# Kernel optimization log

Hardware: AMD Instinct MI355X
Metric: run time of the kernel (lower is better)

Reference implementation:

```python
import jax, jax.numpy as jnp
import numpy as np

N = 4096
IN_F = 512
OUT_F = 64
HEADS = 4
ALPHA = 0.2  # leaky relu slope
NEG_INF = -9e15


def setup_inputs() -> dict:
    key = jax.random.key(0)
    k1, k2, k3, k4 = jax.random.split(key, 4)
    x = jax.random.normal(k1, (N, IN_F), dtype=jnp.float32)
    adj = jax.random.randint(k2, (N, N), 0, 2, dtype=jnp.int32)
    # xavier-uniform-like init for params
    limW = float(np.sqrt(6.0 / (IN_F + OUT_F * HEADS)))
    W = jax.random.uniform(k3, (IN_F, OUT_F * HEADS), dtype=jnp.float32, minval=-limW, maxval=limW)
    lima = float(np.sqrt(6.0 / (2 * OUT_F + 1)))
    a = jax.random.uniform(k4, (2 * OUT_F, 1), dtype=jnp.float32, minval=-lima, maxval=lima)
    return {"x": x, "adj": adj, "W": W, "a": a}


def reference(x, adj, W, a):
    # h: [N, H, F]
    h = (x @ W).reshape(N, HEADS, OUT_F)
    a_src = a[:OUT_F, 0]   # [F]
    a_dst = a[OUT_F:, 0]   # [F]
    s = jnp.einsum("nhf,f->nh", h, a_src)  # source-node score [N, H]
    t = jnp.einsum("nhf,f->nh", h, a_dst)  # dest-node score   [N, H]
    # e[i, j, k] = leaky_relu(s[i,k] + t[j,k]) -> [N, N, H]
    e = jax.nn.leaky_relu(s[:, None, :] + t[None, :, :], negative_slope=ALPHA)
    mask = (adj > 0)[:, :, None]  # [N, N, 1]
    e = jnp.where(mask, e, NEG_INF)
    attn = jax.nn.softmax(e, axis=1)  # softmax over neighbors j
    # weighted aggregation per head: [N, H, F]
    h_prime = jnp.einsum("ijh,jhf->ihf", attn, h)
    return h_prime.reshape(N, HEADS * OUT_F)
```

## Files before the change

### kernel.cpp

```cpp
#include <hip/hip_runtime.h>
#include <hip/hip_bf16.h>


#define NN 4096
#define KF 512
#define NF 256

typedef __attribute__((ext_vector_type(8))) short bf16x8;
typedef __attribute__((ext_vector_type(4))) short s16x4;
typedef __attribute__((ext_vector_type(4))) float f32x4;

union AB8 { bf16x8 v; short2 h[4]; short s[8]; int4 i4; };
union ST4 { s16x4 v; short2 h[2]; };

__device__ __forceinline__ short f2bf(float f) {
    union { float f; unsigned u; } v; v.f = f;
    unsigned r = v.u + 0x7fffu + ((v.u >> 16) & 1u);
    return (short)(r >> 16);
}
__device__ __forceinline__ float bf2f(short b) {
    union { unsigned u; float f; } v;
    v.u = ((unsigned)(unsigned short)b) << 16;
    return v.f;
}
__device__ __forceinline__ short2 pkbf(float a, float b) {
    __hip_bfloat162 t = __float22bfloat162_rn(make_float2(a, b));
    union { __hip_bfloat162 v; short2 s; } u; u.v = t;
    return u.s;
}

__global__ __launch_bounds__(256) void xcast(const float* __restrict__ x,
                                             short* __restrict__ xb) {
    int idx = (blockIdx.x * 256 + threadIdx.x) * 4;
    float4 v = *(const float4*)(x + idx);
    ST4 o; o.h[0] = pkbf(v.x, v.y); o.h[1] = pkbf(v.z, v.w);
    *(s16x4*)(xb + idx) = o.v;
}

__global__ __launch_bounds__(256) void wpack(const float* __restrict__ W,
                                             short* __restrict__ WtF) {
    int tid = blockIdx.x * 256 + threadIdx.x;
    int l = tid & 63, nt = (tid >> 6) & 3, hd = (tid >> 8) & 3, kblk = tid >> 10;
    int q = l >> 4, r = l & 15;
    int col = hd * 64 + nt * 16 + r;
    int k0 = kblk * 32 + q * 8;
    AB8 o;
    #pragma unroll
    for (int e = 0; e < 8; e++) o.s[e] = f2bf(W[(k0 + e) * NF + col]);
    *(bf16x8*)(WtF + (size_t)tid * 8) = o.v;
}

__global__ __launch_bounds__(256) void adjpack(const int* __restrict__ adj,
                                               unsigned* __restrict__ pT) {
    int gw   = (blockIdx.x * 256 + threadIdx.x) >> 6;
    int lane = threadIdx.x & 63;
    int i = gw >> 4, seg = gw & 15;
    const int* ap = adj + (size_t)i * NN + seg * 256 + lane;
    unsigned long long b0 = __ballot(ap[0]   != 0);
    unsigned long long b1 = __ballot(ap[64]  != 0);
    unsigned long long b2 = __ballot(ap[128] != 0);
    unsigned long long b3 = __ballot(ap[192] != 0);
    if (lane == 0) {
        *(uint4*)(pT + ((size_t)(seg * 2    ) * NN + i) * 4) =
            make_uint4((unsigned)b0, (unsigned)(b0 >> 32), (unsigned)b1, (unsigned)(b1 >> 32));
        *(uint4*)(pT + ((size_t)(seg * 2 + 1) * NN + i) * 4) =
            make_uint4((unsigned)b2, (unsigned)(b2 >> 32), (unsigned)b3, (unsigned)(b3 >> 32));
    }
}

__global__ __launch_bounds__(256) void gemm(const short* __restrict__ xb,
                                            const short* __restrict__ WtF,
                                            short* __restrict__ VtF) {
    const int lane = threadIdx.x & 63, wv = threadIdx.x >> 6;
    const int q = lane >> 4, r = lane & 15;
    const int i0 = blockIdx.x * 64 + wv * 16;
    const int hd = blockIdx.y >> 1, ntp = (blockIdx.y & 1) * 2;

    const short* xp = xb + (size_t)(i0 + r) * KF + q * 8;
    const short* wp = WtF + ((size_t)((hd * 4 + ntp) * 64 + lane)) * 8;

    f32x4 acc0 = {}, acc1 = {};
    #pragma unroll
    for (int kb = 0; kb < 16; kb++) {
        bf16x8 av = *(const bf16x8*)(xp + kb * 32);
        bf16x8 b0 = *(const bf16x8*)(wp + kb * 8192);
        bf16x8 b1 = *(const bf16x8*)(wp + kb * 8192 + 512);
        acc0 = __builtin_amdgcn_mfma_f32_16x16x32_bf16(av, b0, acc0, 0, 0, 0);
        acc1 = __builtin_amdgcn_mfma_f32_16x16x32_bf16(av, b1, acc1, 0, 0, 0);
    }
    const int jblk = i0 >> 5;
    const int base = (i0 & 16) + q * 4;
    const int qa = base >> 3, e0 = base & 7;
    ST4 s0, s1;
    s0.h[0] = pkbf(acc0[0], acc0[1]); s0.h[1] = pkbf(acc0[2], acc0[3]);
    s1.h[0] = pkbf(acc1[0], acc1[1]); s1.h[1] = pkbf(acc1[2], acc1[3]);
    *(s16x4*)(VtF + ((size_t)(((jblk * 4 + hd) * 4 + ntp    ) * 64 + qa * 16 + r)) * 8 + e0) = s0.v;
    *(s16x4*)(VtF + ((size_t)(((jblk * 4 + hd) * 4 + ntp + 1) * 64 + qa * 16 + r)) * 8 + e0) = s1.v;
}

__global__ __launch_bounds__(256) void prep(const short* __restrict__ VtF,
                                            const float* __restrict__ a,
                                            float* __restrict__ ipk,
                                            float2* __restrict__ jpk) {
    const int l = threadIdx.x & 63, hd = threadIdx.x >> 6;
    const int q = l >> 4, r = l & 15;
    const int jblk = blockIdx.x;
    float as[4], at[4];
    #pragma unroll
    for (int nt = 0; nt < 4; nt++) { as[nt] = a[nt * 16 + r]; at[nt] = a[64 + nt * 16 + r]; }
    float ps[8] = {}, pt[8] = {};
    #pragma unroll
    for (int nt = 0; nt < 4; nt++) {
        AB8 hv; hv.v = *(const bf16x8*)(VtF + ((size_t)(((jblk * 4 + hd) * 4 + nt) * 64 + l)) * 8);
        #pragma unroll
        for (int e = 0; e < 8; e++) { float v = bf2f(hv.s[e]); ps[e] += v * as[nt]; pt[e] += v * at[nt]; }
    }
    #pragma unroll
    for (int d = 1; d < 16; d <<= 1) {
        #pragma unroll
        for (int e = 0; e < 8; e++) { ps[e] += __shfl_xor(ps[e], d, 64); pt[e] += __shfl_xor(pt[e], d, 64); }
    }
    if (r == 0) {
        #pragma unroll
        for (int e = 0; e < 8; e++) {
            int j = jblk * 32 + q * 8 + e;
            ipk[hd * NN + j] = __expf(-0.8f * ps[e]);
            jpk[hd * NN + j] = make_float2(__expf(pt[e]), __expf(0.2f * pt[e]));
        }
    }
}

struct PF { float4 ja, jb, jc, jd; int4 v0, v1, v2, v3; };

__global__ __launch_bounds__(1024) __attribute__((amdgpu_waves_per_eu(1, 4)))
void gat_attn(const uint4* __restrict__ pT4, const float* __restrict__ ipk,
              const float* __restrict__ jpkf, const short* __restrict__ VtF,
              float* __restrict__ out) {
    const int tid = threadIdx.x, lane = tid & 63, wv = tid >> 6;
    const int hd = wv & 3, jq = wv >> 2;
    const int q = lane >> 4, r = lane & 15;
    const int i0 = blockIdx.x * 16, i = i0 + r;
    const float ci = ipk[hd * NN + i];
    const int qs = q * 8;
    const float* jpf = jpkf + (size_t)hd * NN * 2;

    f32x4 acc[5] = {};
    AB8 ones;
    #pragma unroll
    for (int e = 0; e < 8; e++) ones.s[e] = (short)0x3F80;

    auto load_pf = [&](PF& p, int it) {
        const float4* jp = (const float4*)(jpf + 2 * ((jq << 10) + (it << 5) + qs));
        p.ja = jp[0]; p.jb = jp[1]; p.jc = jp[2]; p.jd = jp[3];
        const int4* vp = (const int4*)(VtF + (size_t)(((jq * 32 + it) * 16 + hd * 4) * 512) + lane * 8);
        p.v0 = vp[0]; p.v1 = vp[64]; p.v2 = vp[128]; p.v3 = vp[192];
    };
    auto consume = [&](const PF& p, unsigned w) {
        float p0 = (w & 1u)   ? fmaxf(p.ja.x, ci * p.ja.y) : 0.f;
        float p1 = (w & 2u)   ? fmaxf(p.ja.z, ci * p.ja.w) : 0.f;
        float p2 = (w & 4u)   ? fmaxf(p.jb.x, ci * p.jb.y) : 0.f;
        float p3 = (w & 8u)   ? fmaxf(p.jb.z, ci * p.jb.w) : 0.f;
        float p4 = (w & 16u)  ? fmaxf(p.jc.x, ci * p.jc.y) : 0.f;
        float p5 = (w & 32u)  ? fmaxf(p.jc.z, ci * p.jc.w) : 0.f;
        float p6 = (w & 64u)  ? fmaxf(p.jd.x, ci * p.jd.y) : 0.f;
        float p7 = (w & 128u) ? fmaxf(p.jd.z, ci * p.jd.w) : 0.f;
        AB8 af;
        af.h[0] = pkbf(p0, p1); af.h[1] = pkbf(p2, p3);
        af.h[2] = pkbf(p4, p5); af.h[3] = pkbf(p6, p7);
        AB8 b0, b1, b2, b3; b0.i4 = p.v0; b1.i4 = p.v1; b2.i4 = p.v2; b3.i4 = p.v3;
        acc[0] = __builtin_amdgcn_mfma_f32_16x16x32_bf16(af.v, b0.v, acc[0], 0, 0, 0);
        acc[1] = __builtin_amdgcn_mfma_f32_16x16x32_bf16(af.v, b1.v, acc[1], 0, 0, 0);
        acc[2] = __builtin_amdgcn_mfma_f32_16x16x32_bf16(af.v, b2.v, acc[2], 0, 0, 0);
        acc[3] = __builtin_amdgcn_mfma_f32_16x16x32_bf16(af.v, b3.v, acc[3], 0, 0, 0);
        acc[4] = __builtin_amdgcn_mfma_f32_16x16x32_bf16(af.v, ones.v, acc[4], 0, 0, 0);
    };

    const uint4* prow = pT4 + (size_t)(jq * 8) * NN + i;
    uint4 wg = prow[0];
    PF pa, pb;
    load_pf(pa, 0);
    #pragma unroll 1
    for (int g = 0; g < 8; g++) {
        uint4 wgn = wg;
        if (g < 7) wgn = prow[(size_t)(g + 1) * NN];
        const int it = g * 4;
        load_pf(pb, it + 1); consume(pa, wg.x >> qs);
        load_pf(pa, it + 2); consume(pb, wg.y >> qs);
        load_pf(pb, it + 3); consume(pa, wg.z >> qs);
        if (g < 7) load_pf(pa, it + 4);
        consume(pb, wg.w >> qs);
        wg = wgn;
    }

    __shared__ float sacc[3][4][5][64][4];
    if (jq > 0) {
        const int gg = jq - 1;
        #pragma unroll
        for (int t = 0; t < 5; t++)
            *(f32x4*)&sacc[gg][hd][t][lane][0] = acc[t];
    }
    __syncthreads();
    if (jq == 0) {
        #pragma unroll
        for (int gg = 0; gg < 3; gg++)
            #pragma unroll
            for (int t = 0; t < 5; t++) {
                f32x4 o = *(const f32x4*)&sacc[gg][hd][t][lane][0];
                acc[t][0] += o[0]; acc[t][1] += o[1];
                acc[t][2] += o[2]; acc[t][3] += o[3];
            }
        #pragma unroll
        for (int reg = 0; reg < 4; reg++) {
            float inv = 1.f / acc[4][reg];
            int row = i0 + q * 4 + reg;
            #pragma unroll
            for (int t = 0; t < 4; t++)
                out[(size_t)row * NF + hd * 64 + t * 16 + r] = acc[t][reg] * inv;
        }
    }
}

extern "C" void kernel_launch(void* const* d_in, const int* in_sizes, int n_in,
                              void* d_out, int out_size, void* d_ws, size_t ws_size,
                              hipStream_t stream) {
    const float* x   = (const float*)d_in[0];
    const int*   adj = (const int*)d_in[1];
    const float* W   = (const float*)d_in[2];
    const float* a   = (const float*)d_in[3];
    float* out = (float*)d_out;

    char* ws = (char*)d_ws;
    short*    xb  = (short*)ws;
    short*    WtF = (short*)(ws + 4194304);
    short*    VtF = (short*)(ws + 4456448);
    unsigned* pT  = (unsigned*)(ws + 6553600);
    float*    ipk = (float*)(ws + 8650752);
    float2*   jpk = (float2*)(ws + 8716288);

    xcast  <<<2048, 256, 0, stream>>>(x, xb);
    wpack  <<<64, 256, 0, stream>>>(W, WtF);
    adjpack<<<16384, 256, 0, stream>>>(adj, pT);
    gemm   <<<dim3(64, 8), 256, 0, stream>>>(xb, WtF, VtF);
    prep   <<<128, 256, 0, stream>>>(VtF, a, ipk, jpk);
    gat_attn<<<256, 1024, 0, stream>>>((const uint4*)pT, ipk, (const float*)jpk, VtF, out);
}
```

Measured before the change: 152.2 us.

## Use FP8 MFMA for attention aggregation and fold x cast into GEMM

```diff
diff --git a/kernel.cpp b/kernel.cpp
--- a/kernel.cpp
+++ b/kernel.cpp
@@ -12,6 +12,7 @@
 
 union AB8 { bf16x8 v; short2 h[4]; short s[8]; int4 i4; };
 union ST4 { s16x4 v; short2 h[2]; };
+union I64 { long v; int i[2]; };
 
 __device__ __forceinline__ short f2bf(float f) {
     union { float f; unsigned u; } v; v.f = f;
@@ -28,13 +29,10 @@
     union { __hip_bfloat162 v; short2 s; } u; u.v = t;
     return u.s;
 }
-
-__global__ __launch_bounds__(256) void xcast(const float* __restrict__ x,
-                                             short* __restrict__ xb) {
-    int idx = (blockIdx.x * 256 + threadIdx.x) * 4;
-    float4 v = *(const float4*)(x + idx);
-    ST4 o; o.h[0] = pkbf(v.x, v.y); o.h[1] = pkbf(v.z, v.w);
-    *(s16x4*)(xb + idx) = o.v;
+__device__ __forceinline__ int pkfp8x4(float a, float b, float c, float d) {
+    int p = __builtin_amdgcn_cvt_pk_fp8_f32(a, b, 0, false);
+    p     = __builtin_amdgcn_cvt_pk_fp8_f32(c, d, p, true);
+    return p;
 }
 
 __global__ __launch_bounds__(256) void wpack(const float* __restrict__ W,
@@ -68,25 +66,30 @@
     }
 }
 
-__global__ __launch_bounds__(256) void gemm(const short* __restrict__ xb,
+__global__ __launch_bounds__(256) void gemm(const float* __restrict__ x,
                                             const short* __restrict__ WtF,
-                                            short* __restrict__ VtF) {
+                                            short* __restrict__ VtF,
+                                            unsigned char* __restrict__ VtF8) {
     const int lane = threadIdx.x & 63, wv = threadIdx.x >> 6;
     const int q = lane >> 4, r = lane & 15;
     const int i0 = blockIdx.x * 64 + wv * 16;
     const int hd = blockIdx.y >> 1, ntp = (blockIdx.y & 1) * 2;
 
-    const short* xp = xb + (size_t)(i0 + r) * KF + q * 8;
+    const float* xp = x + (size_t)(i0 + r) * KF + q * 8;
     const short* wp = WtF + ((size_t)((hd * 4 + ntp) * 64 + lane)) * 8;
 
     f32x4 acc0 = {}, acc1 = {};
-    #pragma unroll
+    #pragma unroll 4
     for (int kb = 0; kb < 16; kb++) {
-        bf16x8 av = *(const bf16x8*)(xp + kb * 32);
+        float4 xa = *(const float4*)(xp + kb * 32);
+        float4 xb2 = *(const float4*)(xp + kb * 32 + 4);
+        AB8 av;
+        av.h[0] = pkbf(xa.x, xa.y);  av.h[1] = pkbf(xa.z, xa.w);
+        av.h[2] = pkbf(xb2.x, xb2.y); av.h[3] = pkbf(xb2.z, xb2.w);
         bf16x8 b0 = *(const bf16x8*)(wp + kb * 8192);
         bf16x8 b1 = *(const bf16x8*)(wp + kb * 8192 + 512);
-        acc0 = __builtin_amdgcn_mfma_f32_16x16x32_bf16(av, b0, acc0, 0, 0, 0);
-        acc1 = __builtin_amdgcn_mfma_f32_16x16x32_bf16(av, b1, acc1, 0, 0, 0);
+        acc0 = __builtin_amdgcn_mfma_f32_16x16x32_bf16(av.v, b0, acc0, 0, 0, 0);
+        acc1 = __builtin_amdgcn_mfma_f32_16x16x32_bf16(av.v, b1, acc1, 0, 0, 0);
     }
     const int jblk = i0 >> 5;
     const int base = (i0 & 16) + q * 4;
@@ -94,8 +97,12 @@
     ST4 s0, s1;
     s0.h[0] = pkbf(acc0[0], acc0[1]); s0.h[1] = pkbf(acc0[2], acc0[3]);
     s1.h[0] = pkbf(acc1[0], acc1[1]); s1.h[1] = pkbf(acc1[2], acc1[3]);
-    *(s16x4*)(VtF + ((size_t)(((jblk * 4 + hd) * 4 + ntp    ) * 64 + qa * 16 + r)) * 8 + e0) = s0.v;
-    *(s16x4*)(VtF + ((size_t)(((jblk * 4 + hd) * 4 + ntp + 1) * 64 + qa * 16 + r)) * 8 + e0) = s1.v;
+    const size_t slot0 = (size_t)(((jblk * 4 + hd) * 4 + ntp    ) * 64 + qa * 16 + r);
+    const size_t slot1 = (size_t)(((jblk * 4 + hd) * 4 + ntp + 1) * 64 + qa * 16 + r);
+    *(s16x4*)(VtF + slot0 * 8 + e0) = s0.v;
+    *(s16x4*)(VtF + slot1 * 8 + e0) = s1.v;
+    *(int*)(VtF8 + slot0 * 8 + e0) = pkfp8x4(acc0[0], acc0[1], acc0[2], acc0[3]);
+    *(int*)(VtF8 + slot1 * 8 + e0) = pkfp8x4(acc1[0], acc1[1], acc1[2], acc1[3]);
 }
 
 __global__ __launch_bounds__(256) void prep(const short* __restrict__ VtF,
@@ -130,11 +137,11 @@
     }
 }
 
-struct PF { float4 ja, jb, jc, jd; int4 v0, v1, v2, v3; };
+struct PF { float4 ja, jb, jc, jd; long v0, v1, v2, v3; };
 
 __global__ __launch_bounds__(1024) __attribute__((amdgpu_waves_per_eu(1, 4)))
 void gat_attn(const uint4* __restrict__ pT4, const float* __restrict__ ipk,
-              const float* __restrict__ jpkf, const short* __restrict__ VtF,
+              const float* __restrict__ jpkf, const unsigned char* __restrict__ VtF8,
               float* __restrict__ out) {
     const int tid = threadIdx.x, lane = tid & 63, wv = tid >> 6;
     const int hd = wv & 3, jq = wv >> 2;
@@ -145,14 +152,12 @@
     const float* jpf = jpkf + (size_t)hd * NN * 2;
 
     f32x4 acc[5] = {};
-    AB8 ones;
-    #pragma unroll
-    for (int e = 0; e < 8; e++) ones.s[e] = (short)0x3F80;
+    const long ones = 0x3838383838383838L;
 
     auto load_pf = [&](PF& p, int it) {
         const float4* jp = (const float4*)(jpf + 2 * ((jq << 10) + (it << 5) + qs));
         p.ja = jp[0]; p.jb = jp[1]; p.jc = jp[2]; p.jd = jp[3];
-        const int4* vp = (const int4*)(VtF + (size_t)(((jq * 32 + it) * 16 + hd * 4) * 512) + lane * 8);
+        const long* vp = (const long*)(VtF8 + (size_t)(((jq * 32 + it) * 16 + hd * 4) * 512) + lane * 8);
         p.v0 = vp[0]; p.v1 = vp[64]; p.v2 = vp[128]; p.v3 = vp[192];
     };
     auto consume = [&](const PF& p, unsigned w) {
@@ -164,15 +169,14 @@
         float p5 = (w & 32u)  ? fmaxf(p.jc.z, ci * p.jc.w) : 0.f;
         float p6 = (w & 64u)  ? fmaxf(p.jd.x, ci * p.jd.y) : 0.f;
         float p7 = (w & 128u) ? fmaxf(p.jd.z, ci * p.jd.w) : 0.f;
-        AB8 af;
-        af.h[0] = pkbf(p0, p1); af.h[1] = pkbf(p2, p3);
-        af.h[2] = pkbf(p4, p5); af.h[3] = pkbf(p6, p7);
-        AB8 b0, b1, b2, b3; b0.i4 = p.v0; b1.i4 = p.v1; b2.i4 = p.v2; b3.i4 = p.v3;
-        acc[0] = __builtin_amdgcn_mfma_f32_16x16x32_bf16(af.v, b0.v, acc[0], 0, 0, 0);
-        acc[1] = __builtin_amdgcn_mfma_f32_16x16x32_bf16(af.v, b1.v, acc[1], 0, 0, 0);
-        acc[2] = __builtin_amdgcn_mfma_f32_16x16x32_bf16(af.v, b2.v, acc[2], 0, 0, 0);
-        acc[3] = __builtin_amdgcn_mfma_f32_16x16x32_bf16(af.v, b3.v, acc[3], 0, 0, 0);
-        acc[4] = __builtin_amdgcn_mfma_f32_16x16x32_bf16(af.v, ones.v, acc[4], 0, 0, 0);
+        I64 af;
+        af.i[0] = pkfp8x4(p0, p1, p2, p3);
+        af.i[1] = pkfp8x4(p4, p5, p6, p7);
+        acc[0] = __builtin_amdgcn_mfma_f32_16x16x32_fp8_fp8(af.v, p.v0, acc[0], 0, 0, 0);
+        acc[1] = __builtin_amdgcn_mfma_f32_16x16x32_fp8_fp8(af.v, p.v1, acc[1], 0, 0, 0);
+        acc[2] = __builtin_amdgcn_mfma_f32_16x16x32_fp8_fp8(af.v, p.v2, acc[2], 0, 0, 0);
+        acc[3] = __builtin_amdgcn_mfma_f32_16x16x32_fp8_fp8(af.v, p.v3, acc[3], 0, 0, 0);
+        acc[4] = __builtin_amdgcn_mfma_f32_16x16x32_fp8_fp8(af.v, ones, acc[4], 0, 0, 0);
     };
 
     const uint4* prow = pT4 + (size_t)(jq * 8) * NN + i;
@@ -230,17 +234,16 @@
     float* out = (float*)d_out;
 
     char* ws = (char*)d_ws;
-    short*    xb  = (short*)ws;
-    short*    WtF = (short*)(ws + 4194304);
-    short*    VtF = (short*)(ws + 4456448);
-    unsigned* pT  = (unsigned*)(ws + 6553600);
-    float*    ipk = (float*)(ws + 8650752);
-    float2*   jpk = (float2*)(ws + 8716288);
-
-    xcast  <<<2048, 256, 0, stream>>>(x, xb);
+    short*         WtF  = (short*)ws;
+    short*         VtF  = (short*)(ws + 262144);
+    unsigned char* VtF8 = (unsigned char*)(ws + 2359296);
+    unsigned*      pT   = (unsigned*)(ws + 3407872);
+    float*         ipk  = (float*)(ws + 5505024);
+    float2*        jpk  = (float2*)(ws + 5570560);
+
     wpack  <<<64, 256, 0, stream>>>(W, WtF);
     adjpack<<<16384, 256, 0, stream>>>(adj, pT);
-    gemm   <<<dim3(64, 8), 256, 0, stream>>>(xb, WtF, VtF);
+    gemm   <<<dim3(64, 8), 256, 0, stream>>>(x, WtF, VtF, VtF8);
     prep   <<<128, 256, 0, stream>>>(VtF, a, ipk, jpk);
-    gat_attn<<<256, 1024, 0, stream>>>((const uint4*)pT, ipk, (const float*)jpk, VtF, out);
-}
+    gat_attn<<<256, 1024, 0, stream>>>((const uint4*)pT, ipk, (const float*)jpk, VtF8, out);
+}
```

Result: no change. 152.7 us (+0.3%).
